# Performance work log

Hardware: AMD Instinct MI355X
Metric: run time of the kernel (lower is better)

The kernel has to match this reference:

```python
import jax, jax.numpy as jnp
import numpy as np

B, N, S, K, H, OBS = 4096, 177, 36, 6, 128, 500
HEADS, FH = 4, 32          # GAT layer1: 4 heads x 32 = 128 concat
C_IN = 3 * H               # [obs_repr | sub_embed | node_embed]


def setup_inputs() -> dict:
    key = jax.random.key(0)
    ks = jax.random.split(key, 16)
    inp = {
        "org_obs": jax.random.normal(ks[0], (B, OBS), jnp.float32),
        "node_embeddings": jax.random.normal(ks[1], (B, N, H), jnp.float32),
        "substation_embeddings": jax.random.normal(ks[2], (B, S, H), jnp.float32),
        "sub_choice": jax.random.randint(ks[3], (B, 1), 0, S),
        "sub_id_to_elem_id": jax.random.randint(ks[4], (S, K), 0, N),
        # org_obs_projection
        "W_proj": jax.random.normal(ks[5], (OBS, H), jnp.float32) * 0.05,
        "b_proj": jnp.zeros((H,), jnp.float32),
        # GAT layer 1: C_IN -> HEADS*FH (concat)
        "W1": jax.random.normal(ks[6], (C_IN, HEADS * FH), jnp.float32) * 0.05,
        "a_src1": jax.random.normal(ks[7], (HEADS, FH), jnp.float32) * 0.05,
        "a_dst1": jax.random.normal(ks[8], (HEADS, FH), jnp.float32) * 0.05,
        "b1": jnp.zeros((HEADS * FH,), jnp.float32),
        # GAT layer 2: HEADS*FH -> 1 (single head)
        "W2": jax.random.normal(ks[9], (HEADS * FH, 1), jnp.float32) * 0.05,
        "a_src2": jax.random.normal(ks[10], (1, 1), jnp.float32) * 0.05,
        "a_dst2": jax.random.normal(ks[11], (1, 1), jnp.float32) * 0.05,
        "b2": jnp.zeros((1,), jnp.float32),
    }
    return inp


def _gat_layer(x, W, a_src, a_dst, b):
    """PyG-style GATConv on a fully-connected graph (with self loops),
    batched over B graphs of K nodes. x: [B,K,Fin]."""
    Bb, Kk, _ = x.shape
    heads, fh = a_src.shape
    h = (x @ W).reshape(Bb, Kk, heads, fh)          # [B,K,heads,fh]
    e_src = jnp.sum(h * a_src, axis=-1)             # [B,K,heads]  a_src . h_j
    e_dst = jnp.sum(h * a_dst, axis=-1)             # [B,K,heads]  a_dst . h_i
    # e[b,i,j,h]: edge j -> i on fully-connected graph
    e = jax.nn.leaky_relu(e_dst[:, :, None, :] + e_src[:, None, :, :], 0.2)
    alpha = jax.nn.softmax(e, axis=2)               # softmax over source j
    out = jnp.einsum('bijh,bjhf->bihf', alpha, h)   # [B,K,heads,fh]
    return out.reshape(Bb, Kk, heads * fh) + b


def reference(org_obs, node_embeddings, substation_embeddings, sub_choice,
              sub_id_to_elem_id, W_proj, b_proj, W1, a_src1, a_dst1, b1,
              W2, a_src2, a_dst2, b2):
    obs_repr = org_obs @ W_proj + b_proj                      # [B,H]
    sub = sub_choice[:, 0]                                    # [B]
    elem_ids = sub_id_to_elem_id[sub]                         # [B,K]
    bidx = jnp.arange(org_obs.shape[0])
    config_nodes = node_embeddings[bidx[:, None], elem_ids]   # [B,K,H] gather
    config_sub = substation_embeddings[bidx, sub]             # [B,H]
    Bb = org_obs.shape[0]
    x = jnp.concatenate([
        jnp.broadcast_to(obs_repr[:, None, :], (Bb, K, H)),
        jnp.broadcast_to(config_sub[:, None, :], (Bb, K, H)),
        config_nodes,
    ], axis=-1)                                               # [B,K,3H]
    h1 = jax.nn.elu(_gat_layer(x, W1, a_src1, a_dst1, b1))    # [B,K,128]
    node_preds = _gat_layer(h1, W2, a_src2, a_dst2, b2)       # [B,K,1]
    return node_preds
```

## Files before the change

### kernel.cpp

```cpp
#include <hip/hip_runtime.h>

#define BB     4096
#define NNODE  177
#define NSUB   36
#define KN     6
#define HH     128
#define OBSD   500
#define TB     16
#define NTHR   512

typedef unsigned short ushort_t;
typedef __attribute__((ext_vector_type(4))) float f32x4;
typedef __attribute__((ext_vector_type(8))) short s16x8;
typedef __attribute__((ext_vector_type(4))) unsigned short u16x4;

#define MFMA16(a, b, c) __builtin_amdgcn_mfma_f32_16x16x32_bf16((a), (b), (c), 0, 0, 0)

__device__ __forceinline__ ushort_t f2bf(float f) {
    unsigned u = __float_as_uint(f);
    u += 0x7FFFu + ((u >> 16) & 1u);
    return (ushort_t)(u >> 16);
}
__device__ __forceinline__ u16x4 f2bf4(float4 v) {
    u16x4 o; o.x = f2bf(v.x); o.y = f2bf(v.y); o.z = f2bf(v.z); o.w = f2bf(v.w);
    return o;
}

__device__ __forceinline__ s16x8 ldB8(const float* __restrict__ W, int k, int col) {
    const float* p = W + k * HH + col;
    float w0 = p[0],      w1 = p[HH],     w2 = p[2 * HH], w3 = p[3 * HH];
    float w4 = p[4 * HH], w5 = p[5 * HH], w6 = p[6 * HH], w7 = p[7 * HH];
    union { unsigned u[4]; s16x8 v; } U;
    asm("v_cvt_pk_bf16_f32 %0, %1, %2" : "=v"(U.u[0]) : "v"(w0), "v"(w1));
    asm("v_cvt_pk_bf16_f32 %0, %1, %2" : "=v"(U.u[1]) : "v"(w2), "v"(w3));
    asm("v_cvt_pk_bf16_f32 %0, %1, %2" : "=v"(U.u[2]) : "v"(w4), "v"(w5));
    asm("v_cvt_pk_bf16_f32 %0, %1, %2" : "=v"(U.u[3]) : "v"(w6), "v"(w7));
    return U.v;
}
__device__ __forceinline__ s16x8 ldB8m(const float* __restrict__ W, int k, int col, int kmax) {
    float w[8];
    #pragma unroll
    for (int j = 0; j < 8; ++j) w[j] = (k + j < kmax) ? W[(k + j) * HH + col] : 0.f;
    union { unsigned u[4]; s16x8 v; } U;
    #pragma unroll
    for (int j = 0; j < 4; ++j)
        asm("v_cvt_pk_bf16_f32 %0, %1, %2" : "=v"(U.u[j]) : "v"(w[2 * j]), "v"(w[2 * j + 1]));
    return U.v;
}

__global__ void __launch_bounds__(NTHR, 2) k_main(
    const float* __restrict__ org_obs, const float* __restrict__ node_emb,
    const float* __restrict__ subst,   const int* __restrict__ sub_choice,
    const int* __restrict__ sub_map,   const float* __restrict__ Wproj,
    const float* __restrict__ bproj,   const float* __restrict__ W1,
    const float* __restrict__ a_src1,  const float* __restrict__ a_dst1,
    const float* __restrict__ b1,      const float* __restrict__ W2,
    const float* __restrict__ a_src2,  const float* __restrict__ a_dst2,
    const float* __restrict__ b2,      float* __restrict__ out) {

    __shared__ __align__(16) char smem[113728];
    float* s_h     = (float*)(smem + 49152);
    float* s_e     = (float*)(smem + 98304);
    float* s_alpha = (float*)(smem + 101376);
    float* s_p     = (float*)(smem + 110656);

    const int t   = threadIdx.x;
    const int gb0 = blockIdx.x * TB;

    float4 nreg[6];
    {
        const int b = t >> 5, l = t & 31;
        const float* orow = org_obs + (size_t)(gb0 + b) * OBSD;
        int sub = sub_choice[gb0 + b];
        const int* emap = sub_map + sub * KN;
        #pragma unroll
        for (int s = 0; s < 6; ++s)
            nreg[s] = ((const float4*)(node_emb +
                        ((size_t)(gb0 + b) * NNODE + emap[s]) * HH))[l];
        const int swz = (b & 7) << 4;
        #pragma unroll
        for (int it = 0; it < 4; ++it) {
            int idx = it * 32 + l;
            u16x4 v = {0, 0, 0, 0};
            if (idx < 125) v = f2bf4(((const float4*)orow)[idx]);
            *(u16x4*)(smem + b * 1280 + ((idx * 8) ^ swz)) = v;
        }
        const float* srow = subst + ((size_t)(gb0 + b) * NSUB + sub) * HH;
        *(u16x4*)(smem + b * 1280 + ((1024 + l * 8) ^ swz)) = f2bf4(((const float4*)srow)[l]);
    }
    __syncthreads();

    const int w = t >> 6, ln = t & 63, r16 = ln & 15, g = ln >> 4;
    const int col = w * 16 + r16;
    const int rswz = (r16 & 7) << 4;

    f32x4 acc1 = {0.f, 0.f, 0.f, 0.f};
    #pragma unroll 5
    for (int kk = 0; kk < 15; ++kk) {
        s16x8 af = *(const s16x8*)(smem + r16 * 1280 + ((kk * 64 + g * 16) ^ rswz));
        s16x8 bf = ldB8(Wproj, kk * 32 + g * 8, col);
        acc1 = MFMA16(af, bf, acc1);
    }
    {
        s16x8 af = *(const s16x8*)(smem + r16 * 1280 + ((15 * 64 + g * 16) ^ rswz));
        s16x8 bf = ldB8m(Wproj, 15 * 32 + g * 8, col, OBSD);
        acc1 = MFMA16(af, bf, acc1);
    }

    {
        float bp = bproj[col];
        #pragma unroll
        for (int rg = 0; rg < 4; ++rg) {
            int bb = g * 4 + rg;
            *(ushort_t*)(smem + 45056 + bb * 256 + ((col * 2) ^ ((bb & 7) << 4))) =
                f2bf(acc1[rg] + bp);
        }
    }
    {
        const int b = t >> 5, l = t & 31;
        const int swz = (b & 7) << 4;
        #pragma unroll
        for (int s = 0; s < 6; ++s)
            *(u16x4*)(smem + 20480 + (s * 16 + b) * 256 + ((l * 8) ^ swz)) =
                f2bf4(nreg[s]);
    }
    __syncthreads();

    f32x4 u2 = {0.f, 0.f, 0.f, 0.f}, acc2 = {0.f, 0.f, 0.f, 0.f};
    #pragma unroll
    for (int kk = 0; kk < 4; ++kk) {
        s16x8 afx = *(const s16x8*)(smem + 45056 + r16 * 256 + ((kk * 64 + g * 16) ^ rswz));
        s16x8 bfx = ldB8(W1, kk * 32 + g * 8, col);
        u2 = MFMA16(afx, bfx, u2);
        s16x8 afs = *(const s16x8*)(smem + r16 * 1280 + ((1024 + kk * 64 + g * 16) ^ rswz));
        s16x8 bfs = ldB8(W1 + 128 * HH, kk * 32 + g * 8, col);
        acc2 = MFMA16(afs, bfs, acc2);
    }

    f32x4 v[6];
    #pragma unroll
    for (int s = 0; s < 6; ++s) v[s] = (f32x4){0.f, 0.f, 0.f, 0.f};
    #pragma unroll
    for (int kk = 0; kk < 4; ++kk) {
        s16x8 bf = ldB8(W1 + 256 * HH, kk * 32 + g * 8, col);
        #pragma unroll
        for (int s = 0; s < 6; ++s) {
            s16x8 af = *(const s16x8*)(smem + 20480 + (s * 16 + r16) * 256 +
                                       ((kk * 64 + g * 16) ^ rswz));
            v[s] = MFMA16(af, bf, v[s]);
        }
    }

    float h[6][4];
    #pragma unroll
    for (int s = 0; s < 6; ++s)
        #pragma unroll
        for (int rg = 0; rg < 4; ++rg) {
            h[s][rg] = u2[rg] + acc2[rg] + v[s][rg];
            s_h[((g * 4 + rg) * 6 + s) * 128 + col] = h[s][rg];
        }
    __syncthreads();

    if (t < 384) {
        int b = t / 24, rem = t - b * 24, i = rem >> 2, hd = rem & 3;
        const float* hrow = s_h + (b * 6 + i) * 128 + hd * 32;
        const float* as = a_src1 + hd * 32;
        const float* ad = a_dst1 + hd * 32;
        float ps = 0.f, pd = 0.f;
        #pragma unroll
        for (int f = 0; f < 32; ++f) {
            float hv = hrow[f];
            ps += hv * as[f];
            pd += hv * ad[f];
        }
        s_e[(b * 6 + i) * 8 + hd]     = ps;
        s_e[(b * 6 + i) * 8 + 4 + hd] = pd;
    }
    __syncthreads();

    if (t < 384) {
        int b = t / 24, rem = t - b * 24, i = rem >> 2, hd = rem & 3;
        float ed = s_e[(b * 6 + i) * 8 + 4 + hd];
        float ev[6], mx = -1e30f;
        #pragma unroll
        for (int j = 0; j < 6; ++j) {
            float e = ed + s_e[(b * 6 + j) * 8 + hd];
            e = (e > 0.f) ? e : 0.2f * e;
            ev[j] = e; mx = fmaxf(mx, e);
        }
        float ex[6], ss = 0.f;
        #pragma unroll
        for (int j = 0; j < 6; ++j) { ex[j] = __expf(ev[j] - mx); ss += ex[j]; }
        float inv = 1.f / ss;
        #pragma unroll
        for (int j = 0; j < 6; ++j)
            s_alpha[b * 145 + i * 24 + hd * 6 + j] = ex[j] * inv;
    }
    __syncthreads();

    {
        const int hd = w >> 1;
        float b1v = b1[col], w2v = W2[col];
        #pragma unroll
        for (int i = 0; i < 6; ++i)
            #pragma unroll
            for (int rg = 0; rg < 4; ++rg) {
                int bb = g * 4 + rg;
                const float* al = s_alpha + bb * 145 + i * 24 + hd * 6;
                float acc = al[0] * h[0][rg] + al[1] * h[1][rg] + al[2] * h[2][rg] +
                            al[3] * h[3][rg] + al[4] * h[4][rg] + al[5] * h[5][rg];
                float o = acc + b1v;
                o = (o > 0.f) ? o : __expf(o) - 1.f;
                float p = o * w2v;
                p += __shfl_xor(p, 1); p += __shfl_xor(p, 2);
                p += __shfl_xor(p, 4); p += __shfl_xor(p, 8);
                if (r16 == 0) s_p[(w * 16 + bb) * 6 + i] = p;
            }
    }
    __syncthreads();

    if (t < 96) {
        int b = t / 6, i = t - b * 6;
        float hh[6];
        #pragma unroll
        for (int j = 0; j < 6; ++j) {
            float acc = 0.f;
            #pragma unroll
            for (int ww = 0; ww < 8; ++ww) acc += s_p[(ww * 16 + b) * 6 + j];
            hh[j] = acc;
        }
        float as2v = a_src2[0], ad2v = a_dst2[0];
        float hi = hh[i];
        float ev[6], mx = -1e30f;
        #pragma unroll
        for (int j = 0; j < 6; ++j) {
            float e = ad2v * hi + as2v * hh[j];
            e = (e > 0.f) ? e : 0.2f * e;
            ev[j] = e; mx = fmaxf(mx, e);
        }
        float ss = 0.f, acc = 0.f;
        #pragma unroll
        for (int j = 0; j < 6; ++j) {
            float ex = __expf(ev[j] - mx);
            ss += ex; acc += ex * hh[j];
        }
        out[(gb0 + b) * 6 + i] = acc / ss + b2[0];
    }
}

extern "C" void kernel_launch(void* const* d_in, const int* in_sizes, int n_in,
                              void* d_out, int out_size, void* d_ws, size_t ws_size,
                              hipStream_t stream) {
    const float* org_obs    = (const float*)d_in[0];
    const float* node_emb   = (const float*)d_in[1];
    const float* subst      = (const float*)d_in[2];
    const int*   sub_choice = (const int*)d_in[3];
    const int*   sub_map    = (const int*)d_in[4];
    const float* Wproj      = (const float*)d_in[5];
    const float* bproj      = (const float*)d_in[6];
    const float* W1         = (const float*)d_in[7];
    const float* a_src1     = (const float*)d_in[8];
    const float* a_dst1     = (const float*)d_in[9];
    const float* b1         = (const float*)d_in[10];
    const float* W2         = (const float*)d_in[11];
    const float* a_src2     = (const float*)d_in[12];
    const float* a_dst2     = (const float*)d_in[13];
    const float* b2         = (const float*)d_in[14];

    hipLaunchKernelGGL(k_main, dim3(BB / TB), dim3(NTHR), 0, stream,
                       org_obs, node_emb, subst, sub_choice, sub_map,
                       Wproj, bproj, W1, a_src1, a_dst1, b1, W2,
                       a_src2, a_dst2, b2, (float*)d_out);
}
```

Before: 23.60 us.

## Process 32 batch rows per block, reusing weight fragments across two M tiles

```diff
diff --git a/kernel.cpp b/kernel.cpp
--- a/kernel.cpp
+++ b/kernel.cpp
@@ -6,7 +6,7 @@
 #define KN     6
 #define HH     128
 #define OBSD   500
-#define TB     16
+#define TB     32
 #define NTHR   512
 
 typedef unsigned short ushort_t;
@@ -58,112 +58,152 @@
     const float* __restrict__ a_src2,  const float* __restrict__ a_dst2,
     const float* __restrict__ b2,      float* __restrict__ out) {
 
-    __shared__ __align__(16) char smem[113728];
-    float* s_h     = (float*)(smem + 49152);
-    float* s_e     = (float*)(smem + 98304);
-    float* s_alpha = (float*)(smem + 101376);
-    float* s_p     = (float*)(smem + 110656);
+    __shared__ __align__(16) char smem[132992];
+    float* s_h     = (float*)smem;
+    float* s_e     = (float*)(smem + 102144);
+    float* s_alpha = (float*)(smem + 108288);
+    float* s_p     = (float*)(smem + 126848);
 
     const int t   = threadIdx.x;
     const int gb0 = blockIdx.x * TB;
 
-    float4 nreg[6];
+    float4 nreg0[6], nreg1[6];
     {
-        const int b = t >> 5, l = t & 31;
+        const int b = t >> 4, l = t & 15;
         const float* orow = org_obs + (size_t)(gb0 + b) * OBSD;
         int sub = sub_choice[gb0 + b];
         const int* emap = sub_map + sub * KN;
         #pragma unroll
-        for (int s = 0; s < 6; ++s)
-            nreg[s] = ((const float4*)(node_emb +
-                        ((size_t)(gb0 + b) * NNODE + emap[s]) * HH))[l];
+        for (int s = 0; s < 6; ++s) {
+            const float4* nrow = (const float4*)(node_emb +
+                ((size_t)(gb0 + b) * NNODE + emap[s]) * HH);
+            nreg0[s] = nrow[l];
+            nreg1[s] = nrow[16 + l];
+        }
         const int swz = (b & 7) << 4;
         #pragma unroll
-        for (int it = 0; it < 4; ++it) {
-            int idx = it * 32 + l;
+        for (int it = 0; it < 8; ++it) {
+            int idx = it * 16 + l;
             u16x4 v = {0, 0, 0, 0};
             if (idx < 125) v = f2bf4(((const float4*)orow)[idx]);
             *(u16x4*)(smem + b * 1280 + ((idx * 8) ^ swz)) = v;
         }
-        const float* srow = subst + ((size_t)(gb0 + b) * NSUB + sub) * HH;
-        *(u16x4*)(smem + b * 1280 + ((1024 + l * 8) ^ swz)) = f2bf4(((const float4*)srow)[l]);
-    }
-    __syncthreads();
+        const float4* srow = (const float4*)(subst + ((size_t)(gb0 + b) * NSUB + sub) * HH);
+        *(u16x4*)(smem + b * 1280 + ((1024 + l * 8) ^ swz)) = f2bf4(srow[l]);
+        *(u16x4*)(smem + b * 1280 + ((1024 + (16 + l) * 8) ^ swz)) = f2bf4(srow[16 + l]);
+    }
 
     const int w = t >> 6, ln = t & 63, r16 = ln & 15, g = ln >> 4;
     const int col = w * 16 + r16;
     const int rswz = (r16 & 7) << 4;
 
-    f32x4 acc1 = {0.f, 0.f, 0.f, 0.f};
-    #pragma unroll 5
-    for (int kk = 0; kk < 15; ++kk) {
-        s16x8 af = *(const s16x8*)(smem + r16 * 1280 + ((kk * 64 + g * 16) ^ rswz));
-        s16x8 bf = ldB8(Wproj, kk * 32 + g * 8, col);
-        acc1 = MFMA16(af, bf, acc1);
-    }
-    {
-        s16x8 af = *(const s16x8*)(smem + r16 * 1280 + ((15 * 64 + g * 16) ^ rswz));
-        s16x8 bf = ldB8m(Wproj, 15 * 32 + g * 8, col, OBSD);
-        acc1 = MFMA16(af, bf, acc1);
+    s16x8 pf0 = ldB8(Wproj, 0 * 32 + g * 8, col);
+    s16x8 pf1 = ldB8(Wproj, 1 * 32 + g * 8, col);
+    s16x8 pf2 = ldB8(Wproj, 2 * 32 + g * 8, col);
+    s16x8 pf3 = ldB8(Wproj, 3 * 32 + g * 8, col);
+    s16x8 pf4 = ldB8(Wproj, 4 * 32 + g * 8, col);
+    s16x8 pf5 = ldB8(Wproj, 5 * 32 + g * 8, col);
+    __syncthreads();
+
+    f32x4 acc1_0 = {0.f, 0.f, 0.f, 0.f}, acc1_1 = {0.f, 0.f, 0.f, 0.f};
+    #pragma unroll
+    for (int kk = 0; kk < 16; ++kk) {
+        s16x8 bf;
+        if      (kk == 0) bf = pf0;
+        else if (kk == 1) bf = pf1;
+        else if (kk == 2) bf = pf2;
+        else if (kk == 3) bf = pf3;
+        else if (kk == 4) bf = pf4;
+        else if (kk == 5) bf = pf5;
+        else if (kk < 15) bf = ldB8(Wproj, kk * 32 + g * 8, col);
+        else              bf = ldB8m(Wproj, kk * 32 + g * 8, col, OBSD);
+        s16x8 af0 = *(const s16x8*)(smem + r16 * 1280 + ((kk * 64 + g * 16) ^ rswz));
+        acc1_0 = MFMA16(af0, bf, acc1_0);
+        s16x8 af1 = *(const s16x8*)(smem + (16 + r16) * 1280 + ((kk * 64 + g * 16) ^ rswz));
+        acc1_1 = MFMA16(af1, bf, acc1_1);
     }
 
     {
         float bp = bproj[col];
         #pragma unroll
         for (int rg = 0; rg < 4; ++rg) {
-            int bb = g * 4 + rg;
-            *(ushort_t*)(smem + 45056 + bb * 256 + ((col * 2) ^ ((bb & 7) << 4))) =
-                f2bf(acc1[rg] + bp);
+            int b0 = g * 4 + rg, b1i = 16 + g * 4 + rg;
+            *(ushort_t*)(smem + 90112 + b0 * 256 + ((col * 2) ^ ((b0 & 7) << 4))) =
+                f2bf(acc1_0[rg] + bp);
+            *(ushort_t*)(smem + 90112 + b1i * 256 + ((col * 2) ^ ((b1i & 7) << 4))) =
+                f2bf(acc1_1[rg] + bp);
         }
     }
     {
-        const int b = t >> 5, l = t & 31;
+        const int b = t >> 4, l = t & 15;
         const int swz = (b & 7) << 4;
         #pragma unroll
-        for (int s = 0; s < 6; ++s)
-            *(u16x4*)(smem + 20480 + (s * 16 + b) * 256 + ((l * 8) ^ swz)) =
-                f2bf4(nreg[s]);
-    }
-    __syncthreads();
-
-    f32x4 u2 = {0.f, 0.f, 0.f, 0.f}, acc2 = {0.f, 0.f, 0.f, 0.f};
+        for (int s = 0; s < 6; ++s) {
+            *(u16x4*)(smem + 40960 + (s * 32 + b) * 256 + ((l * 8) ^ swz)) = f2bf4(nreg0[s]);
+            *(u16x4*)(smem + 40960 + (s * 32 + b) * 256 + (((16 + l) * 8) ^ swz)) = f2bf4(nreg1[s]);
+        }
+    }
+    __syncthreads();
+
+    f32x4 u2[2], ac2[2];
+    #pragma unroll
+    for (int m = 0; m < 2; ++m) { u2[m] = (f32x4){0.f,0.f,0.f,0.f}; ac2[m] = (f32x4){0.f,0.f,0.f,0.f}; }
     #pragma unroll
     for (int kk = 0; kk < 4; ++kk) {
-        s16x8 afx = *(const s16x8*)(smem + 45056 + r16 * 256 + ((kk * 64 + g * 16) ^ rswz));
-        s16x8 bfx = ldB8(W1, kk * 32 + g * 8, col);
-        u2 = MFMA16(afx, bfx, u2);
-        s16x8 afs = *(const s16x8*)(smem + r16 * 1280 + ((1024 + kk * 64 + g * 16) ^ rswz));
-        s16x8 bfs = ldB8(W1 + 128 * HH, kk * 32 + g * 8, col);
-        acc2 = MFMA16(afs, bfs, acc2);
-    }
-
-    f32x4 v[6];
-    #pragma unroll
-    for (int s = 0; s < 6; ++s) v[s] = (f32x4){0.f, 0.f, 0.f, 0.f};
+        s16x8 bfa = ldB8(W1, kk * 32 + g * 8, col);
+        s16x8 bfb = ldB8(W1 + 128 * HH, kk * 32 + g * 8, col);
+        #pragma unroll
+        for (int m = 0; m < 2; ++m) {
+            s16x8 afx = *(const s16x8*)(smem + 90112 + (m * 16 + r16) * 256 +
+                                        ((kk * 64 + g * 16) ^ rswz));
+            u2[m] = MFMA16(afx, bfa, u2[m]);
+            s16x8 afs = *(const s16x8*)(smem + (m * 16 + r16) * 1280 +
+                                        ((1024 + kk * 64 + g * 16) ^ rswz));
+            ac2[m] = MFMA16(afs, bfb, ac2[m]);
+        }
+    }
+
+    f32x4 v[2][6];
+    #pragma unroll
+    for (int m = 0; m < 2; ++m)
+        #pragma unroll
+        for (int s = 0; s < 6; ++s) v[m][s] = (f32x4){0.f, 0.f, 0.f, 0.f};
     #pragma unroll
     for (int kk = 0; kk < 4; ++kk) {
         s16x8 bf = ldB8(W1 + 256 * HH, kk * 32 + g * 8, col);
         #pragma unroll
-        for (int s = 0; s < 6; ++s) {
-            s16x8 af = *(const s16x8*)(smem + 20480 + (s * 16 + r16) * 256 +
-                                       ((kk * 64 + g * 16) ^ rswz));
-            v[s] = MFMA16(af, bf, v[s]);
-        }
-    }
-
-    float h[6][4];
-    #pragma unroll
-    for (int s = 0; s < 6; ++s)
-        #pragma unroll
-        for (int rg = 0; rg < 4; ++rg) {
-            h[s][rg] = u2[rg] + acc2[rg] + v[s][rg];
-            s_h[((g * 4 + rg) * 6 + s) * 128 + col] = h[s][rg];
-        }
-    __syncthreads();
-
-    if (t < 384) {
-        int b = t / 24, rem = t - b * 24, i = rem >> 2, hd = rem & 3;
-        const float* hrow = s_h + (b * 6 + i) * 128 + hd * 32;
+        for (int m = 0; m < 2; ++m)
+            #pragma unroll
+            for (int s = 0; s < 6; ++s) {
+                s16x8 af = *(const s16x8*)(smem + 40960 + (s * 32 + m * 16 + r16) * 256 +
+                                           ((kk * 64 + g * 16) ^ rswz));
+                v[m][s] = MFMA16(af, bf, v[m][s]);
+            }
+    }
+
+    float h[2][6][4];
+    #pragma unroll
+    for (int m = 0; m < 2; ++m)
+        #pragma unroll
+        for (int s = 0; s < 6; ++s)
+            #pragma unroll
+            for (int rg = 0; rg < 4; ++rg)
+                h[m][s][rg] = u2[m][rg] + ac2[m][rg] + v[m][s][rg];
+    __syncthreads();
+    #pragma unroll
+    for (int m = 0; m < 2; ++m)
+        #pragma unroll
+        for (int s = 0; s < 6; ++s)
+            #pragma unroll
+            for (int rg = 0; rg < 4; ++rg) {
+                int bb = m * 16 + g * 4 + rg;
+                s_h[(bb * 6 + s) * 133 + col] = h[m][s][rg];
+            }
+    __syncthreads();
+
+    for (int idx = t; idx < 768; idx += NTHR) {
+        int b = idx / 24, rem = idx - b * 24, i = rem >> 2, hd = rem & 3;
+        const float* hrow = s_h + (b * 6 + i) * 133 + hd * 32;
         const float* as = a_src1 + hd * 32;
         const float* ad = a_dst1 + hd * 32;
         float ps = 0.f, pd = 0.f;
@@ -178,8 +218,8 @@
     }
     __syncthreads();
 
-    if (t < 384) {
-        int b = t / 24, rem = t - b * 24, i = rem >> 2, hd = rem & 3;
+    for (int idx = t; idx < 768; idx += NTHR) {
+        int b = idx / 24, rem = idx - b * 24, i = rem >> 2, hd = rem & 3;
         float ed = s_e[(b * 6 + i) * 8 + 4 + hd];
         float ev[6], mx = -1e30f;
         #pragma unroll
@@ -202,31 +242,34 @@
         const int hd = w >> 1;
         float b1v = b1[col], w2v = W2[col];
         #pragma unroll
-        for (int i = 0; i < 6; ++i)
-            #pragma unroll
-            for (int rg = 0; rg < 4; ++rg) {
-                int bb = g * 4 + rg;
-                const float* al = s_alpha + bb * 145 + i * 24 + hd * 6;
-                float acc = al[0] * h[0][rg] + al[1] * h[1][rg] + al[2] * h[2][rg] +
-                            al[3] * h[3][rg] + al[4] * h[4][rg] + al[5] * h[5][rg];
-                float o = acc + b1v;
-                o = (o > 0.f) ? o : __expf(o) - 1.f;
-                float p = o * w2v;
-                p += __shfl_xor(p, 1); p += __shfl_xor(p, 2);
-                p += __shfl_xor(p, 4); p += __shfl_xor(p, 8);
-                if (r16 == 0) s_p[(w * 16 + bb) * 6 + i] = p;
-            }
-    }
-    __syncthreads();
-
-    if (t < 96) {
+        for (int m = 0; m < 2; ++m)
+            #pragma unroll
+            for (int i = 0; i < 6; ++i)
+                #pragma unroll
+                for (int rg = 0; rg < 4; ++rg) {
+                    int bb = m * 16 + g * 4 + rg;
+                    const float* al = s_alpha + bb * 145 + i * 24 + hd * 6;
+                    float acc = al[0] * h[m][0][rg] + al[1] * h[m][1][rg] +
+                                al[2] * h[m][2][rg] + al[3] * h[m][3][rg] +
+                                al[4] * h[m][4][rg] + al[5] * h[m][5][rg];
+                    float o = acc + b1v;
+                    o = (o > 0.f) ? o : __expf(o) - 1.f;
+                    float p = o * w2v;
+                    p += __shfl_xor(p, 1); p += __shfl_xor(p, 2);
+                    p += __shfl_xor(p, 4); p += __shfl_xor(p, 8);
+                    if (r16 == 0) s_p[(w * 32 + bb) * 6 + i] = p;
+                }
+    }
+    __syncthreads();
+
+    if (t < 192) {
         int b = t / 6, i = t - b * 6;
         float hh[6];
         #pragma unroll
         for (int j = 0; j < 6; ++j) {
             float acc = 0.f;
             #pragma unroll
-            for (int ww = 0; ww < 8; ++ww) acc += s_p[(ww * 16 + b) * 6 + j];
+            for (int ww = 0; ww < 8; ++ww) acc += s_p[(ww * 32 + b) * 6 + j];
             hh[j] = acc;
         }
         float as2v = a_src2[0], ad2v = a_dst2[0];
```

New measurement: 31.65 us. +34.1%, slower.
